# Performance work log

Measured on AMD Instinct MI355X. Metric: run time of the kernel, lower is better.

The kernel has to match this reference:

```python
import jax, jax.numpy as jnp
import numpy as np

N_NODES = 100000
N_EDGES = 1600000
F_IN, F_HID, F_OUT = 128, 256, 128


def setup_inputs() -> dict:
    key = jax.random.key(0)
    ks = jax.random.split(key, 9)
    x = jax.random.normal(ks[0], (N_NODES, F_IN), dtype=jnp.float32)
    edge_src = jax.random.randint(ks[1], (N_EDGES,), 0, N_NODES, dtype=jnp.int32)
    edge_dst = jax.random.randint(ks[2], (N_EDGES,), 0, N_NODES, dtype=jnp.int32)
    s1 = 1.0 / np.sqrt(F_IN)
    s2 = 1.0 / np.sqrt(F_HID)
    W_self1 = jax.random.uniform(ks[3], (F_IN, F_HID), jnp.float32, -s1, s1)
    W_neigh1 = jax.random.uniform(ks[4], (F_IN, F_HID), jnp.float32, -s1, s1)
    b1 = jnp.zeros((F_HID,), jnp.float32)
    W_self2 = jax.random.uniform(ks[5], (F_HID, F_OUT), jnp.float32, -s2, s2)
    W_neigh2 = jax.random.uniform(ks[6], (F_HID, F_OUT), jnp.float32, -s2, s2)
    b2 = jnp.zeros((F_OUT,), jnp.float32)
    return {"x": x, "edge_src": edge_src, "edge_dst": edge_dst,
            "W_self1": W_self1, "W_neigh1": W_neigh1, "b1": b1,
            "W_self2": W_self2, "W_neigh2": W_neigh2, "b2": b2}


def _sage_mean(h, src, dst, W_self, W_neigh, b):
    # mean-aggregate neighbor features onto dst nodes (DGL SAGEConv 'mean')
    deg = jax.ops.segment_sum(jnp.ones_like(src, dtype=h.dtype), dst,
                              num_segments=N_NODES)
    neigh_sum = jax.ops.segment_sum(h[src], dst, num_segments=N_NODES)
    neigh = neigh_sum / jnp.maximum(deg, 1.0)[:, None]
    return h @ W_self + neigh @ W_neigh + b


def reference(x, edge_src, edge_dst, W_self1, W_neigh1, b1, W_self2, W_neigh2, b2):
    h = _sage_mean(x, edge_src, edge_dst, W_self1, W_neigh1, b1)
    h = jax.nn.sigmoid(h)
    h = _sage_mean(h, edge_src, edge_dst, W_self2, W_neigh2, b2)
    return h
```

## Files before the change

kernel.cpp:

```cpp
#include <hip/hip_runtime.h>
#include <hip/hip_bf16.h>

#define N_NODES 100000
#define N_EDGES 1600000
#define F_IN 128
#define F_HID 256
#define F_OUT 128

typedef unsigned short ushort_t;
typedef __attribute__((ext_vector_type(4))) float f32x4;
typedef __attribute__((ext_vector_type(8))) short bf16x8;

#define GAS __attribute__((address_space(1)))
#define LAS __attribute__((address_space(3)))

__device__ __forceinline__ float bf2f(ushort_t u) {
    unsigned int x = ((unsigned int)u) << 16;
    return __builtin_bit_cast(float, x);
}
__device__ __forceinline__ ushort_t f2bf(float f) {
    unsigned int x = __builtin_bit_cast(unsigned int, f);
    unsigned int r = (x + 0x7fffu + ((x >> 16) & 1u)) >> 16;
    return (ushort_t)r;
}

#define NBUCK ((N_NODES + 255) >> 8)
#define CHUNK 4096

__global__ __launch_bounds__(256) void bucket_count_kernel(
    const int* __restrict__ dst, int* __restrict__ bucket_cnt, int n) {
    __shared__ int hist[NBUCK];
    int tid = threadIdx.x;
    int e0 = blockIdx.x * CHUNK;
    int cnt = n - e0; if (cnt > CHUNK) cnt = CHUNK;
    for (int b = tid; b < NBUCK; b += 256) hist[b] = 0;
    __syncthreads();
    for (int i = tid; i < cnt; i += 256) {
        int d = __builtin_nontemporal_load(dst + e0 + i);
        atomicAdd(&hist[d >> 8], 1);
    }
    __syncthreads();
    for (int b = tid; b < NBUCK; b += 256)
        if (hist[b]) atomicAdd(&bucket_cnt[b], hist[b]);
}

__global__ __launch_bounds__(512) void bucket_scan_kernel(
    const int* __restrict__ bucket_cnt, int* __restrict__ bbase,
    int* __restrict__ bcursor, int* __restrict__ rowptr) {
    __shared__ int tmp[512];
    int tid = threadIdx.x;
    int v = (tid < NBUCK) ? bucket_cnt[tid] : 0;
    tmp[tid] = v;
    __syncthreads();
#pragma unroll
    for (int off = 1; off < 512; off <<= 1) {
        int t = (tid >= off) ? tmp[tid - off] : 0;
        __syncthreads();
        tmp[tid] += t;
        __syncthreads();
    }
    if (tid < NBUCK) {
        int base = tmp[tid] - v;
        bbase[tid] = base;
        bcursor[tid] = base;
    }
    if (tid == 0) {
        bbase[NBUCK] = N_EDGES;
        rowptr[N_NODES] = N_EDGES;
    }
}

__global__ __launch_bounds__(256) void bin_edges_kernel(
    const int* __restrict__ src, const int* __restrict__ dst,
    int* __restrict__ bcursor, unsigned int* __restrict__ pairs, int n) {
    __shared__ int sdst[CHUNK];
    __shared__ int ssrc[CHUNK];
    __shared__ int hist[NBUCK];
    __shared__ int resv[NBUCK];
    int tid = threadIdx.x;
    int e0 = blockIdx.x * CHUNK;
    int cnt = n - e0; if (cnt > CHUNK) cnt = CHUNK;
    for (int b = tid; b < NBUCK; b += 256) hist[b] = 0;
    __syncthreads();
    for (int i = tid; i < cnt; i += 256) {
        int d = __builtin_nontemporal_load(dst + e0 + i);
        int s = __builtin_nontemporal_load(src + e0 + i);
        sdst[i] = d;
        ssrc[i] = s;
        atomicAdd(&hist[d >> 8], 1);
    }
    __syncthreads();
    for (int b = tid; b < NBUCK; b += 256) {
        int h = hist[b];
        resv[b] = h ? atomicAdd(&bcursor[b], h) : 0;
        hist[b] = 0;
    }
    __syncthreads();
    for (int i = tid; i < cnt; i += 256) {
        int d = sdst[i], s = ssrc[i];
        int b = d >> 8;
        int off = atomicAdd(&hist[b], 1);
        pairs[resv[b] + off] = ((unsigned)(d & 255) << 17) | (unsigned)s;
    }
}

__global__ __launch_bounds__(256) void sort_bucket_kernel(
    const unsigned int* __restrict__ pairs, const int* __restrict__ bbase,
    int* __restrict__ rowptr, float* __restrict__ invdeg,
    int* __restrict__ csr_src, int nNodes) {
    __shared__ int lcnt[256];
    __shared__ int lrp[256];
    int tid = threadIdx.x;
    int base = blockIdx.x << 8;
    int nn = nNodes - base; if (nn > 256) nn = 256;
    lcnt[tid] = 0;
    __syncthreads();
    int e0 = bbase[blockIdx.x], e1 = bbase[blockIdx.x + 1];
    for (int i = e0 + tid; i < e1; i += 256)
        atomicAdd(&lcnt[pairs[i] >> 17], 1);
    __syncthreads();
    int v = lcnt[tid];
    lrp[tid] = v;
    __syncthreads();
#pragma unroll
    for (int off = 1; off < 256; off <<= 1) {
        int t = (tid >= off) ? lrp[tid - off] : 0;
        __syncthreads();
        lrp[tid] += t;
        __syncthreads();
    }
    lcnt[tid] = 0;
    lrp[tid] = lrp[tid] - v + e0;
    if (tid < nn) {
        rowptr[base + tid] = lrp[tid];
        invdeg[base + tid] = 1.0f / fmaxf((float)v, 1.0f);
    }
    __syncthreads();
    for (int i = e0 + tid; i < e1; i += 256) {
        unsigned pv = pairs[i];
        int j = (int)(pv >> 17);
        int off = atomicAdd(&lcnt[j], 1);
        csr_src[lrp[j] + off] = (int)(pv & 0x1FFFFu);
    }
}

__global__ __launch_bounds__(256) void convert_x_kernel(const float* __restrict__ x,
                                                        ushort_t* __restrict__ xb, int n4) {
    int i = blockIdx.x * 256 + threadIdx.x;
    if (i >= n4) return;
    int e = i * 4;
    f32x4 v = __builtin_nontemporal_load((const f32x4*)(x + e));
    ushort4 o;
    o.x = f2bf(v.x); o.y = f2bf(v.y); o.z = f2bf(v.z); o.w = f2bf(v.w);
    *(ushort4*)(xb + e) = o;
}

__global__ __launch_bounds__(256) void wtransK_kernel(const float* __restrict__ W1,
                                                      const float* __restrict__ W2,
                                                      ushort_t* __restrict__ Wt,
                                                      int Kx, int Ktot, int N) {
    int i = blockIdx.x * 256 + threadIdx.x;
    if (i >= N * Ktot) return;
    int n = i / Ktot, k = i - n * Ktot;
    float v = (k < Kx) ? W1[(size_t)k * N + n] : W2[(size_t)(k - Kx) * N + n];
    Wt[(size_t)n * Ktot + k] = f2bf(v);
}

__global__ __launch_bounds__(256) void wtransN_kernel(const float* __restrict__ Wa,
                                                      const float* __restrict__ Wb,
                                                      ushort_t* __restrict__ Wt,
                                                      int K, int Nh) {
    int i = blockIdx.x * 256 + threadIdx.x;
    if (i >= 2 * Nh * K) return;
    int n = i / K, k = i - n * K;
    const float* W = (n < Nh) ? Wa : Wb;
    int nn = (n < Nh) ? n : n - Nh;
    Wt[(size_t)n * K + k] = f2bf(W[(size_t)k * Nh + nn]);
}

#define ACC8(arr, v)                                                \
    arr[0] += bf2f((ushort_t)((v).x & 0xffffu));                    \
    arr[1] += bf2f((ushort_t)((v).x >> 16));                        \
    arr[2] += bf2f((ushort_t)((v).y & 0xffffu));                    \
    arr[3] += bf2f((ushort_t)((v).y >> 16));                        \
    arr[4] += bf2f((ushort_t)((v).z & 0xffffu));                    \
    arr[5] += bf2f((ushort_t)((v).z >> 16));                        \
    arr[6] += bf2f((ushort_t)((v).w & 0xffffu));                    \
    arr[7] += bf2f((ushort_t)((v).w >> 16));

template <int MODE>
__global__ __launch_bounds__(256) void gather2_kernel(
    const ushort_t* __restrict__ H,
    const int* __restrict__ rowptr,
    const int* __restrict__ csr_src,
    const float* __restrict__ invdeg,
    const ushort_t* __restrict__ uself,
    const float* __restrict__ bias,
    void* __restrict__ outp,
    int nNodes, int totWaves) {
    int lane = threadIdx.x & 63;
    int wv = blockIdx.x * 4 + (threadIdx.x >> 6);
    int grp = lane >> 4, sub = lane & 15;
    const size_t cofs = (size_t)sub * 8;
    int pair = wv;
    if (pair * 2 >= nNodes) return;
    int r0 = rowptr[pair * 2];
    int r1 = rowptr[pair * 2 + 1];
    int r2 = rowptr[pair * 2 + 2];
    while (true) {
        int npair = pair + totWaves;
        bool hasNext = (npair * 2 < nNodes);
        int n0 = 0, n1 = 0, n2 = 0;
        if (hasNext) {
            n0 = rowptr[npair * 2];
            n1 = rowptr[npair * 2 + 1];
            n2 = rowptr[npair * 2 + 2];
        }
        int nodeA = pair * 2;
        int sA = r0, eA = r1, sB = r1, eB = r2;
        int cA = sA < N_EDGES ? sA : N_EDGES - 1;
        int cB = sB < N_EDGES ? sB : N_EDGES - 1;
        float accA[8] = {}, accB[8] = {};
        for (int ea = sA + grp, eb = sB + grp; ea < eA || eb < eB; ea += 16, eb += 16) {
            bool pa0 = ea < eA, pa1 = ea + 4 < eA, pa2 = ea + 8 < eA, pa3 = ea + 12 < eA;
            bool pb0 = eb < eB, pb1 = eb + 4 < eB, pb2 = eb + 8 < eB, pb3 = eb + 12 < eB;
            int ja0 = pa0 ? ea : cA, ja1 = pa1 ? ea + 4 : cA;
            int ja2 = pa2 ? ea + 8 : cA, ja3 = pa3 ? ea + 12 : cA;
            int jb0 = pb0 ? eb : cB, jb1 = pb1 ? eb + 4 : cB;
            int jb2 = pb2 ? eb + 8 : cB, jb3 = pb3 ? eb + 12 : cB;
            int sa0 = csr_src[ja0], sa1 = csr_src[ja1];
            int sa2 = csr_src[ja2], sa3 = csr_src[ja3];
            int sb0 = csr_src[jb0], sb1 = csr_src[jb1];
            int sb2 = csr_src[jb2], sb3 = csr_src[jb3];
            uint4 va0 = *(const uint4*)(H + (size_t)sa0 * 128 + cofs);
            uint4 va1 = *(const uint4*)(H + (size_t)sa1 * 128 + cofs);
            uint4 va2 = *(const uint4*)(H + (size_t)sa2 * 128 + cofs);
            uint4 va3 = *(const uint4*)(H + (size_t)sa3 * 128 + cofs);
            uint4 vb0 = *(const uint4*)(H + (size_t)sb0 * 128 + cofs);
            uint4 vb1 = *(const uint4*)(H + (size_t)sb1 * 128 + cofs);
            uint4 vb2 = *(const uint4*)(H + (size_t)sb2 * 128 + cofs);
            uint4 vb3 = *(const uint4*)(H + (size_t)sb3 * 128 + cofs);
            if (pa0) { ACC8(accA, va0); }
            if (pa1) { ACC8(accA, va1); }
            if (pa2) { ACC8(accA, va2); }
            if (pa3) { ACC8(accA, va3); }
            if (pb0) { ACC8(accB, vb0); }
            if (pb1) { ACC8(accB, vb1); }
            if (pb2) { ACC8(accB, vb2); }
            if (pb3) { ACC8(accB, vb3); }
        }
#pragma unroll
        for (int j = 0; j < 8; ++j) {
            accA[j] += __shfl_xor(accA[j], 16);
            accA[j] += __shfl_xor(accA[j], 32);
            accB[j] += __shfl_xor(accB[j], 16);
            accB[j] += __shfl_xor(accB[j], 32);
        }
        if (grp == 0) {
            int nodeB = nodeA + 1;
            float scA = invdeg[nodeA];
            float scB = (nodeB < nNodes) ? invdeg[nodeB] : 1.0f;
            if (MODE == 0) {
                uint4 o;
                o.x = (unsigned)f2bf(accA[0] * scA) | ((unsigned)f2bf(accA[1] * scA) << 16);
                o.y = (unsigned)f2bf(accA[2] * scA) | ((unsigned)f2bf(accA[3] * scA) << 16);
                o.z = (unsigned)f2bf(accA[4] * scA) | ((unsigned)f2bf(accA[5] * scA) << 16);
                o.w = (unsigned)f2bf(accA[6] * scA) | ((unsigned)f2bf(accA[7] * scA) << 16);
                *(uint4*)((ushort_t*)outp + (size_t)nodeA * 128 + cofs) = o;
                if (nodeB < nNodes) {
                    uint4 p2;
                    p2.x = (unsigned)f2bf(accB[0] * scB) | ((unsigned)f2bf(accB[1] * scB) << 16);
                    p2.y = (unsigned)f2bf(accB[2] * scB) | ((unsigned)f2bf(accB[3] * scB) << 16);
                    p2.z = (unsigned)f2bf(accB[4] * scB) | ((unsigned)f2bf(accB[5] * scB) << 16);
                    p2.w = (unsigned)f2bf(accB[6] * scB) | ((unsigned)f2bf(accB[7] * scB) << 16);
                    *(uint4*)((ushort_t*)outp + (size_t)nodeB * 128 + cofs) = p2;
                }
            } else {
                uint4 us = *(const uint4*)(uself + (size_t)nodeA * 128 + cofs);
                f32x4 o0, o1;
                o0.x = accA[0] * scA + bf2f((ushort_t)(us.x & 0xffffu)) + bias[cofs + 0];
                o0.y = accA[1] * scA + bf2f((ushort_t)(us.x >> 16)) + bias[cofs + 1];
                o0.z = accA[2] * scA + bf2f((ushort_t)(us.y & 0xffffu)) + bias[cofs + 2];
                o0.w = accA[3] * scA + bf2f((ushort_t)(us.y >> 16)) + bias[cofs + 3];
                o1.x = accA[4] * scA + bf2f((ushort_t)(us.z & 0xffffu)) + bias[cofs + 4];
                o1.y = accA[5] * scA + bf2f((ushort_t)(us.z >> 16)) + bias[cofs + 5];
                o1.z = accA[6] * scA + bf2f((ushort_t)(us.w & 0xffffu)) + bias[cofs + 6];
                o1.w = accA[7] * scA + bf2f((ushort_t)(us.w >> 16)) + bias[cofs + 7];
                float* op = (float*)outp + (size_t)nodeA * 128 + cofs;
                __builtin_nontemporal_store(o0, (f32x4*)op);
                __builtin_nontemporal_store(o1, (f32x4*)(op + 4));
                if (nodeB < nNodes) {
                    uint4 u2 = *(const uint4*)(uself + (size_t)nodeB * 128 + cofs);
                    f32x4 q0, q1;
                    q0.x = accB[0] * scB + bf2f((ushort_t)(u2.x & 0xffffu)) + bias[cofs + 0];
                    q0.y = accB[1] * scB + bf2f((ushort_t)(u2.x >> 16)) + bias[cofs + 1];
                    q0.z = accB[2] * scB + bf2f((ushort_t)(u2.y & 0xffffu)) + bias[cofs + 2];
                    q0.w = accB[3] * scB + bf2f((ushort_t)(u2.y >> 16)) + bias[cofs + 3];
                    q1.x = accB[4] * scB + bf2f((ushort_t)(u2.z & 0xffffu)) + bias[cofs + 4];
                    q1.y = accB[5] * scB + bf2f((ushort_t)(u2.z >> 16)) + bias[cofs + 5];
                    q1.z = accB[6] * scB + bf2f((ushort_t)(u2.w & 0xffffu)) + bias[cofs + 6];
                    q1.w = accB[7] * scB + bf2f((ushort_t)(u2.w >> 16)) + bias[cofs + 7];
                    float* oq = (float*)outp + (size_t)nodeB * 128 + cofs;
                    __builtin_nontemporal_store(q0, (f32x4*)oq);
                    __builtin_nontemporal_store(q1, (f32x4*)(oq + 4));
                }
            }
        }
        if (!hasNext) break;
        pair = npair; r0 = n0; r1 = n1; r2 = n2;
    }
}

__global__ __launch_bounds__(256) void gemm_mfma_kernel(
    const ushort_t* __restrict__ A1, int lda1,
    const ushort_t* __restrict__ A2, int lda2, int Kx,
    const ushort_t* __restrict__ Bt,
    const float* __restrict__ bias,
    ushort_t* __restrict__ CoutA, int ldcA,
    ushort_t* __restrict__ CoutB, int ldcB,
    int M, int mode) {
    __shared__ ushort_t shmem[2 * 128 * 64];
    ushort_t* As = shmem;
    ushort_t* Bs = shmem + 128 * 64;
    int tid = threadIdx.x;
    int lane = tid & 63, wid = tid >> 6;
    int l15 = lane & 15, kgrp = lane >> 4, l7 = lane & 7, l8 = lane >> 3;
    int bm = blockIdx.x * 128, bn = blockIdx.y * 128;
    int wr = (wid >> 1) * 64, wc = (wid & 1) * 64;

    f32x4 acc[4][4] = {};

    for (int k0 = 0; k0 < 256; k0 += 64) {
        const ushort_t* Ap = (k0 < Kx) ? A1 : A2;
        int lda = (k0 < Kx) ? lda1 : lda2;
        int kk0 = (k0 < Kx) ? k0 : k0 - Kx;
#pragma unroll
        for (int t = 0; t < 4; ++t) {
            int c = wid * 4 + t;
            int row = c * 8 + l8;
            int scol = ((l7 ^ (row & 7)) << 3);
            int ar = bm + row; if (ar > M - 1) ar = M - 1;
            __builtin_amdgcn_global_load_lds(
                (const GAS void*)(Ap + (size_t)ar * lda + kk0 + scol),
                (LAS void*)(&As[c * 512]), 16, 0, 0);
            int br = bn + row;
            __builtin_amdgcn_global_load_lds(
                (const GAS void*)(Bt + (size_t)br * 256 + k0 + scol),
                (LAS void*)(&Bs[c * 512]), 16, 0, 0);
        }
        __syncthreads();
#pragma unroll
        for (int kk = 0; kk < 2; ++kk) {
            bf16x8 af[4], bfv[4];
#pragma unroll
            for (int mi = 0; mi < 4; ++mi) {
                int row = wr + mi * 16 + l15;
                int kel = (kk * 32 + kgrp * 8) ^ ((row & 7) << 3);
                af[mi] = *(const bf16x8*)(&As[row * 64 + kel]);
            }
#pragma unroll
            for (int ni = 0; ni < 4; ++ni) {
                int row = wc + ni * 16 + l15;
                int kel = (kk * 32 + kgrp * 8) ^ ((row & 7) << 3);
                bfv[ni] = *(const bf16x8*)(&Bs[row * 64 + kel]);
            }
#pragma unroll
            for (int mi = 0; mi < 4; ++mi)
#pragma unroll
                for (int ni = 0; ni < 4; ++ni)
                    acc[mi][ni] = __builtin_amdgcn_mfma_f32_16x16x32_bf16(
                        af[mi], bfv[ni], acc[mi][ni], 0, 0, 0);
        }
        __syncthreads();
    }

    ushort_t* my = shmem + wid * 4096;
#pragma unroll
    for (int mi = 0; mi < 4; ++mi) {
#pragma unroll
        for (int ni = 0; ni < 4; ++ni) {
            int gcol = bn + wc + ni * 16 + l15;
#pragma unroll
            for (int r = 0; r < 4; ++r) {
                float v = acc[mi][ni][r];
                if (mode == 0) {
                    v += bias[gcol];
                    v = 1.0f / (1.0f + __expf(-v));
                }
                int lr = mi * 16 + kgrp * 4 + r;
                int lc = (ni * 16 + l15) ^ (kgrp << 3);
                my[lr * 64 + lc] = f2bf(v);
            }
        }
    }
#pragma unroll
    for (int it = 0; it < 8; ++it) {
        int r2 = (lane >> 3) + it * 8;
        int swz = ((r2 >> 2) & 3) << 3;
        int c2 = ((lane & 7) << 3) ^ swz;
        bf16x8 vv = *(const bf16x8*)(&my[r2 * 64 + c2]);
        int grow = bm + wr + r2;
        if (grow < M) {
            int gc = bn + wc + (c2 ^ swz);
            ushort_t* dstp = (gc < 128)
                ? CoutA + (size_t)grow * ldcA + gc
                : CoutB + (size_t)grow * ldcB + (gc - 128);
            *(bf16x8*)dstp = vv;
        }
    }
}

extern "C" void kernel_launch(void* const* d_in, const int* in_sizes, int n_in,
                              void* d_out, int out_size, void* d_ws, size_t ws_size,
                              hipStream_t stream) {
    const float* x        = (const float*)d_in[0];
    const int*   src      = (const int*)d_in[1];
    const int*   dst      = (const int*)d_in[2];
    const float* W_self1  = (const float*)d_in[3];
    const float* W_neigh1 = (const float*)d_in[4];
    const float* b1       = (const float*)d_in[5];
    const float* W_self2  = (const float*)d_in[6];
    const float* W_neigh2 = (const float*)d_in[7];
    const float* b2       = (const float*)d_in[8];
    float* out = (float*)d_out;

    char* p = (char*)d_ws;
    auto alloc = [&](size_t bytes) { char* r = p; p += (bytes + 255) & ~(size_t)255; return r; };
    float*    invdeg   = (float*)alloc((size_t)N_NODES * 4);
    ushort_t* xb       = (ushort_t*)alloc((size_t)N_NODES * 128 * 2);
    ushort_t* agg      = (ushort_t*)alloc((size_t)N_NODES * 128 * 2);
    ushort_t* h        = (ushort_t*)alloc((size_t)N_NODES * 256 * 2);
    ushort_t* uself    = (ushort_t*)alloc((size_t)N_NODES * 128 * 2);
    ushort_t* uneigh   = (ushort_t*)alloc((size_t)N_NODES * 128 * 2);
    ushort_t* Wt1      = (ushort_t*)alloc((size_t)256 * 256 * 2);
    ushort_t* Wt2      = (ushort_t*)alloc((size_t)256 * 256 * 2);
    int* rowptr        = (int*)alloc((size_t)(N_NODES + 1) * 4);
    int* bucket_cnt    = (int*)alloc((size_t)NBUCK * 4);
    int* bbase         = (int*)alloc((size_t)(NBUCK + 1) * 4);
    int* bcursor       = (int*)alloc((size_t)NBUCK * 4);
    unsigned int* pairs= (unsigned int*)alloc((size_t)N_EDGES * 4);
    int* csr_src       = (int*)alloc((size_t)N_EDGES * 4);

    convert_x_kernel<<<(N_NODES * F_IN / 4 + 255) / 256, 256, 0, stream>>>(
        x, xb, N_NODES * F_IN / 4);
    wtransK_kernel<<<(256 * 256 + 255) / 256, 256, 0, stream>>>(
        W_self1, W_neigh1, Wt1, 128, 256, 256);
    wtransN_kernel<<<(256 * 256 + 255) / 256, 256, 0, stream>>>(
        W_self2, W_neigh2, Wt2, 256, 128);

    hipMemsetAsync(bucket_cnt, 0, (size_t)NBUCK * sizeof(int), stream);
    bucket_count_kernel<<<(N_EDGES + CHUNK - 1) / CHUNK, 256, 0, stream>>>(
        dst, bucket_cnt, N_EDGES);
    bucket_scan_kernel<<<1, 512, 0, stream>>>(bucket_cnt, bbase, bcursor, rowptr);
    bin_edges_kernel<<<(N_EDGES + CHUNK - 1) / CHUNK, 256, 0, stream>>>(
        src, dst, bcursor, pairs, N_EDGES);
    sort_bucket_kernel<<<NBUCK, 256, 0, stream>>>(
        pairs, bbase, rowptr, invdeg, csr_src, N_NODES);

    const int GATHER_BLOCKS = 2048;
    const int TOT_WAVES = GATHER_BLOCKS * 4;

    gather2_kernel<0><<<GATHER_BLOCKS, 256, 0, stream>>>(
        xb, rowptr, csr_src, invdeg, nullptr, nullptr, agg, N_NODES, TOT_WAVES);
    {
        dim3 grid((N_NODES + 127) / 128, 2);
        gemm_mfma_kernel<<<grid, 256, 0, stream>>>(
            xb, 128, agg, 128, 128, Wt1, b1, h, 256, h + 128, 256, N_NODES, 0);
    }

    {
        dim3 grid((N_NODES + 127) / 128, 2);
        gemm_mfma_kernel<<<grid, 256, 0, stream>>>(
            h, 256, h, 256, 256, Wt2, nullptr, uself, 128, uneigh, 128, N_NODES, 1);
    }
    gather2_kernel<1><<<GATHER_BLOCKS, 256, 0, stream>>>(
        uneigh, rowptr, csr_src, invdeg, uself, b2, out, N_NODES, TOT_WAVES);
}
```

Measured before the change: 292.5 us.

## Double-buffer GEMM K-tiles and compute full 256-column output per 512-thread block

The MFMA GEMM now uses 512-thread blocks covering all 256 output columns, so each A row tile is loaded once instead of twice across a 2-wide grid. The K loop is split into 32-wide stages with double-buffered LDS and global_load_lds prefetch of the next stage overlapping the current MFMAs. The epilogue is restructured to stage and write one 16-row sub-tile at a time within a smaller per-wave LDS region. This increases LDS per block and halves the block count, which may affect occupancy.

New measurement: 282.9 us. 3.3% less time.

```diff
diff --git a/kernel.cpp b/kernel.cpp
--- a/kernel.cpp
+++ b/kernel.cpp
@@ -311,7 +311,7 @@
     }
 }
 
-__global__ __launch_bounds__(256) void gemm_mfma_kernel(
+__global__ __launch_bounds__(512) void gemm_mfma_kernel(
     const ushort_t* __restrict__ A1, int lda1,
     const ushort_t* __restrict__ A2, int lda2, int Kx,
     const ushort_t* __restrict__ Bt,
@@ -319,67 +319,73 @@
     ushort_t* __restrict__ CoutA, int ldcA,
     ushort_t* __restrict__ CoutB, int ldcB,
     int M, int mode) {
-    __shared__ ushort_t shmem[2 * 128 * 64];
-    ushort_t* As = shmem;
-    ushort_t* Bs = shmem + 128 * 64;
+    __shared__ ushort_t shmem[2 * 128 * 32 + 2 * 256 * 32];
+    ushort_t* Asb[2] = {shmem, shmem + 4096};
+    ushort_t* Bsb[2] = {shmem + 8192, shmem + 16384};
     int tid = threadIdx.x;
     int lane = tid & 63, wid = tid >> 6;
-    int l15 = lane & 15, kgrp = lane >> 4, l7 = lane & 7, l8 = lane >> 3;
-    int bm = blockIdx.x * 128, bn = blockIdx.y * 128;
-    int wr = (wid >> 1) * 64, wc = (wid & 1) * 64;
-
-    f32x4 acc[4][4] = {};
-
-    for (int k0 = 0; k0 < 256; k0 += 64) {
+    int l15 = lane & 15, kgrp = lane >> 4;
+    int bm = blockIdx.x * 128;
+    int wr = (wid >> 2) * 64, wc = (wid & 3) * 64;
+
+    auto stage = [&](int buf, int t) {
+        int k0 = t * 32;
         const ushort_t* Ap = (k0 < Kx) ? A1 : A2;
         int lda = (k0 < Kx) ? lda1 : lda2;
         int kk0 = (k0 < Kx) ? k0 : k0 - Kx;
-#pragma unroll
-        for (int t = 0; t < 4; ++t) {
-            int c = wid * 4 + t;
-            int row = c * 8 + l8;
-            int scol = ((l7 ^ (row & 7)) << 3);
+        {
+            int row = wid * 16 + (lane >> 2);
+            int scol = ((lane & 3) ^ (row & 3)) << 3;
             int ar = bm + row; if (ar > M - 1) ar = M - 1;
             __builtin_amdgcn_global_load_lds(
                 (const GAS void*)(Ap + (size_t)ar * lda + kk0 + scol),
-                (LAS void*)(&As[c * 512]), 16, 0, 0);
-            int br = bn + row;
+                (LAS void*)(&Asb[buf][wid * 512]), 16, 0, 0);
+        }
+#pragma unroll
+        for (int t2 = 0; t2 < 2; ++t2) {
+            int c = wid * 2 + t2;
+            int row = c * 16 + (lane >> 2);
+            int scol = ((lane & 3) ^ (row & 3)) << 3;
             __builtin_amdgcn_global_load_lds(
-                (const GAS void*)(Bt + (size_t)br * 256 + k0 + scol),
-                (LAS void*)(&Bs[c * 512]), 16, 0, 0);
-        }
+                (const GAS void*)(Bt + (size_t)row * 256 + k0 + scol),
+                (LAS void*)(&Bsb[buf][c * 512]), 16, 0, 0);
+        }
+    };
+
+    f32x4 acc[4][4] = {};
+
+    stage(0, 0);
+    __syncthreads();
+#pragma unroll
+    for (int t = 0; t < 8; ++t) {
+        int buf = t & 1;
+        if (t < 7) stage(buf ^ 1, t + 1);
+        bf16x8 af[4], bfv[4];
+#pragma unroll
+        for (int mi = 0; mi < 4; ++mi) {
+            int row = wr + mi * 16 + l15;
+            af[mi] = *(const bf16x8*)(&Asb[buf][row * 32 + ((kgrp ^ (row & 3)) << 3)]);
+        }
+#pragma unroll
+        for (int ni = 0; ni < 4; ++ni) {
+            int row = wc + ni * 16 + l15;
+            bfv[ni] = *(const bf16x8*)(&Bsb[buf][row * 32 + ((kgrp ^ (row & 3)) << 3)]);
+        }
+#pragma unroll
+        for (int mi = 0; mi < 4; ++mi)
+#pragma unroll
+            for (int ni = 0; ni < 4; ++ni)
+                acc[mi][ni] = __builtin_amdgcn_mfma_f32_16x16x32_bf16(
+                    af[mi], bfv[ni], acc[mi][ni], 0, 0, 0);
         __syncthreads();
-#pragma unroll
-        for (int kk = 0; kk < 2; ++kk) {
-            bf16x8 af[4], bfv[4];
-#pragma unroll
-            for (int mi = 0; mi < 4; ++mi) {
-                int row = wr + mi * 16 + l15;
-                int kel = (kk * 32 + kgrp * 8) ^ ((row & 7) << 3);
-                af[mi] = *(const bf16x8*)(&As[row * 64 + kel]);
-            }
-#pragma unroll
-            for (int ni = 0; ni < 4; ++ni) {
-                int row = wc + ni * 16 + l15;
-                int kel = (kk * 32 + kgrp * 8) ^ ((row & 7) << 3);
-                bfv[ni] = *(const bf16x8*)(&Bs[row * 64 + kel]);
-            }
-#pragma unroll
-            for (int mi = 0; mi < 4; ++mi)
-#pragma unroll
-                for (int ni = 0; ni < 4; ++ni)
-                    acc[mi][ni] = __builtin_amdgcn_mfma_f32_16x16x32_bf16(
-                        af[mi], bfv[ni], acc[mi][ni], 0, 0, 0);
-        }
-        __syncthreads();
-    }
-
-    ushort_t* my = shmem + wid * 4096;
+    }
+
+    ushort_t* my = shmem + wid * 1024;
 #pragma unroll
     for (int mi = 0; mi < 4; ++mi) {
 #pragma unroll
         for (int ni = 0; ni < 4; ++ni) {
-            int gcol = bn + wc + ni * 16 + l15;
+            int gcol = wc + ni * 16 + l15;
 #pragma unroll
             for (int r = 0; r < 4; ++r) {
                 float v = acc[mi][ni][r];
@@ -387,25 +393,25 @@
                     v += bias[gcol];
                     v = 1.0f / (1.0f + __expf(-v));
                 }
-                int lr = mi * 16 + kgrp * 4 + r;
+                int lr = kgrp * 4 + r;
                 int lc = (ni * 16 + l15) ^ (kgrp << 3);
                 my[lr * 64 + lc] = f2bf(v);
             }
         }
-    }
-#pragma unroll
-    for (int it = 0; it < 8; ++it) {
-        int r2 = (lane >> 3) + it * 8;
-        int swz = ((r2 >> 2) & 3) << 3;
-        int c2 = ((lane & 7) << 3) ^ swz;
-        bf16x8 vv = *(const bf16x8*)(&my[r2 * 64 + c2]);
-        int grow = bm + wr + r2;
-        if (grow < M) {
-            int gc = bn + wc + (c2 ^ swz);
-            ushort_t* dstp = (gc < 128)
-                ? CoutA + (size_t)grow * ldcA + gc
-                : CoutB + (size_t)grow * ldcB + (gc - 128);
-            *(bf16x8*)dstp = vv;
+#pragma unroll
+        for (int it = 0; it < 2; ++it) {
+            int r2 = (lane >> 3) + it * 8;
+            int swz = ((r2 >> 2) & 3) << 3;
+            int c2 = ((lane & 7) << 3) ^ swz;
+            bf16x8 vv = *(const bf16x8*)(&my[r2 * 64 + c2]);
+            int grow = bm + wr + mi * 16 + r2;
+            if (grow < M) {
+                int gc = wc + (c2 ^ swz);
+                ushort_t* dstp = (gc < 128)
+                    ? CoutA + (size_t)grow * ldcA + gc
+                    : CoutB + (size_t)grow * ldcB + (gc - 128);
+                *(bf16x8*)dstp = vv;
+            }
         }
     }
 }
@@ -463,14 +469,14 @@
     gather2_kernel<0><<<GATHER_BLOCKS, 256, 0, stream>>>(
         xb, rowptr, csr_src, invdeg, nullptr, nullptr, agg, N_NODES, TOT_WAVES);
     {
-        dim3 grid((N_NODES + 127) / 128, 2);
-        gemm_mfma_kernel<<<grid, 256, 0, stream>>>(
+        dim3 grid((N_NODES + 127) / 128);
+        gemm_mfma_kernel<<<grid, 512, 0, stream>>>(
             xb, 128, agg, 128, 128, Wt1, b1, h, 256, h + 128, 256, N_NODES, 0);
     }
 
     {
-        dim3 grid((N_NODES + 127) / 128, 2);
-        gemm_mfma_kernel<<<grid, 256, 0, stream>>>(
+        dim3 grid((N_NODES + 127) / 128);
+        gemm_mfma_kernel<<<grid, 512, 0, stream>>>(
             h, 256, h, 256, 256, Wt2, nullptr, uself, 128, uneigh, 128, N_NODES, 1);
     }
     gather2_kernel<1><<<GATHER_BLOCKS, 256, 0, stream>>>(
```
